# Optimization experiments

Measured on AMD Instinct MI355X. Metric: run time of the kernel, lower is better.

## Reference

```python
import jax, jax.numpy as jnp
import numpy as np

B, C, H, W = 16, 64, 192, 192
P, L = 128, 512  # num_paths, max path length


def setup_inputs() -> dict:
    key = jax.random.key(0)
    k1, k2, k3 = jax.random.split(key, 3)
    features = jax.random.normal(k1, (B, C, H, W), dtype=jnp.float32)
    # flattened (r*W + c) coordinates per path step (stand-in for A* paths)
    path_idx = jax.random.randint(k2, (B, P, L), 0, H * W, dtype=jnp.int64)
    W_m = jax.random.normal(k3, (C, C), dtype=jnp.float32) / np.sqrt(C)
    b_m = jnp.zeros((C,), dtype=jnp.float32)
    return {"features": features, "path_idx": path_idx, "W_m": W_m, "b_m": b_m}


def reference(features, path_idx, W_m, b_m):
    Bc, Cc, Hc, Wc = features.shape
    HW = Hc * Wc
    # [B, HW, C] layout for per-pixel gather (feat_map[r, c] in the original)
    feat_hw = features.reshape(Bc, Cc, HW).transpose(0, 2, 1)
    idx = path_idx.reshape(Bc, -1)  # [B, P*L]
    # gather path features: path_features[p, step] = feat_map[r, c]
    gathered = jnp.take_along_axis(feat_hw, idx[..., None], axis=1)  # [B, P*L, C]
    # mamba_corrector stand-in: per-step linear transform
    mamba_out = gathered @ W_m + b_m  # [B, P*L, C]

    def scatter_one(i, v):
        corr = jnp.zeros((HW, Cc), v.dtype).at[i].add(v)
        cnt = jnp.zeros((HW,), v.dtype).at[i].add(jnp.ones_like(i, v.dtype))
        return corr, cnt

    corr, cnt = jax.vmap(scatter_one)(idx, mamba_out)  # [B,HW,C], [B,HW]
    corr = corr / jnp.clip(cnt, 1.0)[..., None]  # counts.clamp(min=1)
    return corr.transpose(0, 2, 1).reshape(Bc, Cc, Hc, Wc)
```

## Files before the change

### kernel.cpp

```cpp
#include <hip/hip_runtime.h>

#define B_    16
#define C_    64
#define HDIM  192
#define WDIM  192
#define HW    (HDIM * WDIM)
#define P_    128
#define L_    512
#define STEPS (P_ * L_)

__global__ __launch_bounds__(256) void touch_kernel(const int* __restrict__ idx,
                                                    unsigned char* __restrict__ mask) {
    int t = blockIdx.x * blockDim.x + threadIdx.x;
    const int4 v = ((const int4*)idx)[t];
    int b = (t * 4) >> 16;
    unsigned char* mb = mask + (size_t)b * HW;
    mb[v.x] = 1;
    mb[v.y] = 1;
    mb[v.z] = 1;
    mb[v.w] = 1;
}

__global__ __launch_bounds__(256) void mm_mask_kernel(const float* __restrict__ feat,
                                                      const float* __restrict__ Wm,
                                                      const float* __restrict__ bm,
                                                      const unsigned char* __restrict__ mask,
                                                      float* __restrict__ out) {
    __shared__ float ldsF[C_ * 64];

    const int t     = threadIdx.x;
    const int blk   = blockIdx.x;
    const int b     = blk / (HW / 64);
    const int chunk = blk % (HW / 64);
    const int hw0   = chunk * 64;

    const float* fbase = feat + (size_t)b * C_ * HW + hw0;
#pragma unroll
    for (int r = 0; r < 4; ++r) {
        int id = r * 256 + t;
        int c  = id >> 4;
        int q  = id & 15;
        float4 v = *(const float4*)(fbase + (size_t)c * HW + q * 4);
        *(float4*)(&ldsF[c * 64 + q * 4]) = v;
    }
    __syncthreads();

    const int px = t & 63;
    const int c0 = __builtin_amdgcn_readfirstlane((t >> 6) * 16);

    float acc[16];
#pragma unroll
    for (int i = 0; i < 16; ++i) acc[i] = bm[c0 + i];

#pragma unroll
    for (int kb = 0; kb < C_; kb += 4) {
        float f[4];
#pragma unroll
        for (int j = 0; j < 4; ++j) f[j] = ldsF[(kb + j) * 64 + px];
#pragma unroll
        for (int j = 0; j < 4; ++j) {
            const float* wrow = Wm + (kb + j) * C_ + c0;
#pragma unroll
            for (int i = 0; i < 16; ++i) acc[i] += f[j] * wrow[i];
        }
    }

    const float msk = mask[(size_t)b * HW + hw0 + px] ? 1.0f : 0.0f;
    float* obase = out + (size_t)b * C_ * HW + hw0 + px;
#pragma unroll
    for (int i = 0; i < 16; ++i)
        obase[(size_t)(c0 + i) * HW] = acc[i] * msk;
}

extern "C" void kernel_launch(void* const* d_in, const int* in_sizes, int n_in,
                              void* d_out, int out_size, void* d_ws, size_t ws_size,
                              hipStream_t stream) {
    const float*         feat = (const float*)d_in[0];
    const int*           idx  = (const int*)d_in[1];
    const float*         Wm   = (const float*)d_in[2];
    const float*         bm   = (const float*)d_in[3];
    float*               out  = (float*)d_out;
    unsigned char*       mask = (unsigned char*)d_ws;

    hipMemsetAsync(mask, 0, (size_t)B_ * HW, stream);

    const int touch_threads = (B_ * STEPS) / 4;
    touch_kernel<<<touch_threads / 256, 256, 0, stream>>>(idx, mask);

    mm_mask_kernel<<<B_ * (HW / 64), 256, 0, stream>>>(feat, Wm, bm, mask, out);
}
```

Baseline: 289.1 us.

## Use LDS bitmask for touched pixels and packed two-pixel matmul

The touch kernel now builds a per-block bitmask in shared memory with atomicOr and merges it into a global bit-packed mask. This replaces a million scattered byte stores to global memory and shrinks the mask memset. The transform kernel now handles 128 pixels per block and 2 pixels per thread using float2 vectors. That lets the compiler use packed FMAs and 8-byte stores, and halves the per-pixel weight loads, at the cost of more registers. Global atomics on the merged mask add some contention.

New measurement: 290.7 us. Within noise of the previous version (+0.5%).

```diff
diff --git a/kernel.cpp b/kernel.cpp
--- a/kernel.cpp
+++ b/kernel.cpp
@@ -2,90 +2,116 @@
 
 #define B_    16
 #define C_    64
-#define HDIM  192
-#define WDIM  192
-#define HW    (HDIM * WDIM)
-#define P_    128
-#define L_    512
-#define STEPS (P_ * L_)
+#define HW    36864
+#define STEPS 65536
+#define NBM   (HW / 32)
+#define SPLIT 16
+#define PXT   128
+
+typedef float f2 __attribute__((ext_vector_type(2)));
 
 __global__ __launch_bounds__(256) void touch_kernel(const int* __restrict__ idx,
-                                                    unsigned char* __restrict__ mask) {
-    int t = blockIdx.x * blockDim.x + threadIdx.x;
-    const int4 v = ((const int4*)idx)[t];
-    int b = (t * 4) >> 16;
-    unsigned char* mb = mask + (size_t)b * HW;
-    mb[v.x] = 1;
-    mb[v.y] = 1;
-    mb[v.z] = 1;
-    mb[v.w] = 1;
+                                                    unsigned int* __restrict__ gmask) {
+    __shared__ unsigned int lm[NBM];
+    const int t   = threadIdx.x;
+    const int blk = blockIdx.x;
+    const int b   = blk >> 4;
+    const int s   = blk & 15;
+
+    for (int i = t; i < NBM; i += 256) lm[i] = 0u;
+    __syncthreads();
+
+    const int4* p = (const int4*)idx + ((b * STEPS + s * (STEPS / SPLIT)) >> 2);
+#pragma unroll
+    for (int k = 0; k < 4; ++k) {
+        int4 v = p[k * 256 + t];
+        atomicOr(&lm[v.x >> 5], 1u << (v.x & 31));
+        atomicOr(&lm[v.y >> 5], 1u << (v.y & 31));
+        atomicOr(&lm[v.z >> 5], 1u << (v.z & 31));
+        atomicOr(&lm[v.w >> 5], 1u << (v.w & 31));
+    }
+    __syncthreads();
+
+    unsigned int* g = gmask + b * NBM;
+    for (int i = t; i < NBM; i += 256) {
+        unsigned int m = lm[i];
+        if (m) atomicOr(&g[i], m);
+    }
 }
 
 __global__ __launch_bounds__(256) void mm_mask_kernel(const float* __restrict__ feat,
                                                       const float* __restrict__ Wm,
                                                       const float* __restrict__ bm,
-                                                      const unsigned char* __restrict__ mask,
+                                                      const unsigned int* __restrict__ gmask,
                                                       float* __restrict__ out) {
-    __shared__ float ldsF[C_ * 64];
+    __shared__ float ldsF[C_ * PXT];
 
-    const int t     = threadIdx.x;
-    const int blk   = blockIdx.x;
-    const int b     = blk / (HW / 64);
-    const int chunk = blk % (HW / 64);
-    const int hw0   = chunk * 64;
+    const int t   = threadIdx.x;
+    const int blk = blockIdx.x;
+    const int b   = blk / (HW / PXT);
+    const int hw0 = (blk % (HW / PXT)) * PXT;
 
     const float* fbase = feat + (size_t)b * C_ * HW + hw0;
 #pragma unroll
-    for (int r = 0; r < 4; ++r) {
+    for (int r = 0; r < 8; ++r) {
         int id = r * 256 + t;
-        int c  = id >> 4;
-        int q  = id & 15;
+        int c  = id >> 5;
+        int q  = id & 31;
         float4 v = *(const float4*)(fbase + (size_t)c * HW + q * 4);
-        *(float4*)(&ldsF[c * 64 + q * 4]) = v;
+        *(float4*)(&ldsF[c * PXT + q * 4]) = v;
     }
     __syncthreads();
 
-    const int px = t & 63;
+    const int l  = t & 63;
     const int c0 = __builtin_amdgcn_readfirstlane((t >> 6) * 16);
 
-    float acc[16];
+    f2 acc[16];
 #pragma unroll
-    for (int i = 0; i < 16; ++i) acc[i] = bm[c0 + i];
+    for (int i = 0; i < 16; ++i) { float bv = bm[c0 + i]; acc[i] = (f2){bv, bv}; }
 
+    const f2* lds2 = (const f2*)ldsF;
 #pragma unroll
     for (int kb = 0; kb < C_; kb += 4) {
-        float f[4];
+        f2 f[4];
 #pragma unroll
-        for (int j = 0; j < 4; ++j) f[j] = ldsF[(kb + j) * 64 + px];
+        for (int j = 0; j < 4; ++j) f[j] = lds2[(kb + j) * (PXT / 2) + l];
 #pragma unroll
         for (int j = 0; j < 4; ++j) {
             const float* wrow = Wm + (kb + j) * C_ + c0;
 #pragma unroll
-            for (int i = 0; i < 16; ++i) acc[i] += f[j] * wrow[i];
+            for (int i = 0; i < 16; ++i) {
+                float w = wrow[i];
+                acc[i] += f[j] * (f2){w, w};
+            }
         }
     }
 
-    const float msk = mask[(size_t)b * HW + hw0 + px] ? 1.0f : 0.0f;
-    float* obase = out + (size_t)b * C_ * HW + hw0 + px;
+    unsigned int m = gmask[b * NBM + (hw0 >> 5) + (l >> 4)];
+    const int sh = (2 * l) & 31;
+    f2 msk = (f2){ ((m >> sh) & 1u) ? 1.0f : 0.0f,
+                   ((m >> (sh + 1)) & 1u) ? 1.0f : 0.0f };
+
+    float* obase = out + (size_t)b * C_ * HW + hw0 + 2 * l;
 #pragma unroll
-    for (int i = 0; i < 16; ++i)
-        obase[(size_t)(c0 + i) * HW] = acc[i] * msk;
+    for (int i = 0; i < 16; ++i) {
+        f2 r = acc[i] * msk;
+        *(f2*)(obase + (size_t)(c0 + i) * HW) = r;
+    }
 }
 
 extern "C" void kernel_launch(void* const* d_in, const int* in_sizes, int n_in,
                               void* d_out, int out_size, void* d_ws, size_t ws_size,
                               hipStream_t stream) {
-    const float*         feat = (const float*)d_in[0];
-    const int*           idx  = (const int*)d_in[1];
-    const float*         Wm   = (const float*)d_in[2];
-    const float*         bm   = (const float*)d_in[3];
-    float*               out  = (float*)d_out;
-    unsigned char*       mask = (unsigned char*)d_ws;
+    const float*   feat  = (const float*)d_in[0];
+    const int*     idx   = (const int*)d_in[1];
+    const float*   Wm    = (const float*)d_in[2];
+    const float*   bm    = (const float*)d_in[3];
+    float*         out   = (float*)d_out;
+    unsigned int*  gmask = (unsigned int*)d_ws;
 
-    hipMemsetAsync(mask, 0, (size_t)B_ * HW, stream);
+    hipMemsetAsync(gmask, 0, (size_t)B_ * NBM * sizeof(unsigned int), stream);
 
-    const int touch_threads = (B_ * STEPS) / 4;
-    touch_kernel<<<touch_threads / 256, 256, 0, stream>>>(idx, mask);
+    touch_kernel<<<B_ * SPLIT, 256, 0, stream>>>(idx, gmask);
 
-    mm_mask_kernel<<<B_ * (HW / 64), 256, 0, stream>>>(feat, Wm, bm, mask, out);
+    mm_mask_kernel<<<B_ * (HW / PXT), 256, 0, stream>>>(feat, Wm, bm, gmask, out);
 }
```
